# Kernel tuning notes

Measured on AMD Instinct MI355X. Metric: run time of the kernel, lower is better.

The kernel has to match this reference:

```python
import jax, jax.numpy as jnp
import numpy as np

B = 16384
D_VIS, D_LANG, D_STATE = 768, 768, 64
D = 256          # d_model
E = 4            # n_experts
K = 2            # top_k
D_IN = D_VIS + D_LANG + D_STATE
EPS = 1e-5


def layernorm(x, g, b):
    mu = x.mean(-1, keepdims=True)
    var = ((x - mu) ** 2).mean(-1, keepdims=True)
    return g * (x - mu) / jnp.sqrt(var + EPS) + b


def setup_inputs() -> dict:
    key = jax.random.key(0)
    ks = jax.random.split(key, 16)
    s = 0.02
    return {
        "vis": jax.random.normal(ks[0], (B, D_VIS), jnp.float32),
        "lang": jax.random.normal(ks[1], (B, D_LANG), jnp.float32),
        "state": jax.random.normal(ks[2], (B, D_STATE), jnp.float32),
        # fusion: Linear(d_in, d_model) + LayerNorm
        "Wf": jax.random.normal(ks[3], (D_IN, D), jnp.float32) * s,
        "bf": jnp.zeros((D,), jnp.float32),
        "gf": jnp.ones((D,), jnp.float32),
        "bfln": jnp.zeros((D,), jnp.float32),
        # gate (bias=False); random instead of zeros so routing is nontrivial
        "Wg": jax.random.normal(ks[4], (D, E), jnp.float32) * s,
        # stacked experts: Linear(d,2d) -> GELU -> Linear(2d,d) -> GELU -> Linear(d,d), then LN(x + net(x))
        "W1": jax.random.normal(ks[5], (E, D, 2 * D), jnp.float32) * s,
        "b1": jnp.zeros((E, 2 * D), jnp.float32),
        "W2": jax.random.normal(ks[6], (E, 2 * D, D), jnp.float32) * s,
        "b2": jnp.zeros((E, D), jnp.float32),
        "W3": jax.random.normal(ks[7], (E, D, D), jnp.float32) * s,
        "b3": jnp.zeros((E, D), jnp.float32),
        "eg": jnp.ones((E, D), jnp.float32),
        "eb": jnp.zeros((E, D), jnp.float32),
    }


def reference(vis, lang, state, Wf, bf, gf, bfln, Wg, W1, b1, W2, b2, W3, b3, eg, eb):
    gelu = lambda t: jax.nn.gelu(t, approximate=False)
    # fusion: Linear -> LayerNorm -> GELU  (dropout is eval-mode identity)
    x = jnp.concatenate([vis, lang, state], axis=-1) @ Wf + bf   # [B, D]
    x = gelu(layernorm(x, gf, bfln))

    logits = x @ Wg                                              # [B, E]
    all_probs = jax.nn.softmax(logits, axis=-1)
    top_vals, top_idx = jax.lax.top_k(logits, K)                 # [B, K]
    top_w = jax.nn.softmax(top_vals, axis=-1)                    # [B, K]

    # all experts densely (E small); original computes same math per masked subset
    h = gelu(jnp.einsum('bd,edh->beh', x, W1) + b1)              # [B, E, 2D]
    h = gelu(jnp.einsum('beh,ehd->bed', h, W2) + b2)             # [B, E, D]
    h = jnp.einsum('bed,edf->bef', h, W3) + b3                   # [B, E, D]
    y = layernorm(x[:, None, :] + h, eg, eb)                     # [B, E, D]

    # gather selected experts and combine with top-k weights
    y_sel = jnp.take_along_axis(y, top_idx[:, :, None], axis=1)  # [B, K, D]
    out = jnp.einsum('bk,bkd->bd', top_w, y_sel)                 # [B, D]

    # load-balance loss: importance x load
    counts = jnp.zeros((E,), x.dtype).at[top_idx.reshape(-1)].add(1.0)
    f_i = counts / (B * K)
    lb_loss = E * jnp.sum(f_i * all_probs.mean(0))
    return out, lb_loss
```

## Files before the change

### kernel.cpp

```cpp
#include <hip/hip_runtime.h>
#include <math.h>


typedef unsigned short u16;
typedef unsigned int u32;
typedef __attribute__((ext_vector_type(8))) short bf16x8;
typedef __attribute__((ext_vector_type(4))) float f32x4;

__device__ __forceinline__ float bf2f(u16 u) {
    union { u32 i; float f; } v; v.i = ((u32)u) << 16; return v.f;
}
__device__ __forceinline__ u16 f2bf(float f) {
    union { float f; u32 i; } v; v.f = f;
    u32 x = v.i;
    return (u16)((x + 0x7fffu + ((x >> 16) & 1u)) >> 16);
}
__device__ __forceinline__ float gelu_fast(float x) {
    float t = x * (1.59576912f + 0.07135481f * x * x);
    return x / (1.f + __expf(-t));
}
__device__ __forceinline__ u32 pk2(u32 f0, u32 f1) {
    return __builtin_amdgcn_perm(f1, f0, 0x07060302);
}

typedef __attribute__((address_space(1))) void GV;
typedef __attribute__((address_space(3))) void SV;
__device__ __forceinline__ void gldlds(const void* g, void* l) {
    __builtin_amdgcn_global_load_lds((GV*)g, (SV*)l, 16, 0, 0);
}

#define SEG_WF  409600
#define SEG_W1  524288
#define SEG_W2  524288
#define SEG_W3  262144
#define PREP_ITEMS (SEG_WF + SEG_W1 + SEG_W2 + SEG_W3 + 8)

__global__ __launch_bounds__(256) void prep_kernel(
    const float* __restrict__ Wf, const float* __restrict__ W1, const float* __restrict__ W2,
    const float* __restrict__ W3,
    u16* __restrict__ wft, u16* __restrict__ w1t, u16* __restrict__ w2t, u16* __restrict__ w3t,
    float* __restrict__ lbacc) {
    int idx = blockIdx.x * 256 + threadIdx.x;
    if (idx < SEG_WF) {
        int n = idx / 1600, k = idx % 1600;
        wft[idx] = f2bf(Wf[(size_t)k * 256 + n]);
        return;
    }
    idx -= SEG_WF;
    if (idx < SEG_W1) {
        int e = idx >> 17, r = idx & 131071;
        int n = r >> 8, k = r & 255;
        w1t[idx] = f2bf(W1[(size_t)e * 131072 + (size_t)k * 512 + n]);
        return;
    }
    idx -= SEG_W1;
    if (idx < SEG_W2) {
        int e = idx >> 17, r = idx & 131071;
        int n = r >> 9, k = r & 511;
        w2t[idx] = f2bf(W2[(size_t)e * 131072 + (size_t)k * 256 + n]);
        return;
    }
    idx -= SEG_W2;
    if (idx < SEG_W3) {
        int e = idx >> 16, r = idx & 65535;
        int n = r >> 8, k = r & 255;
        w3t[idx] = f2bf(W3[(size_t)e * 65536 + (size_t)k * 256 + n]);
        return;
    }
    idx -= SEG_W3;
    if (idx < 8) lbacc[idx] = 0.0f;
}

__global__ __launch_bounds__(256) void fusion_kernel(
    const float* __restrict__ vis, const float* __restrict__ lang, const float* __restrict__ state,
    const u16* __restrict__ BT, const float* __restrict__ bfv_, const float* __restrict__ gf,
    const float* __restrict__ bfln, const float* __restrict__ Wg,
    u16* __restrict__ xbf, float* __restrict__ wr, float* __restrict__ lbacc) {
    __shared__ __align__(16) u32 Af[2][2048];
    __shared__ __align__(16) u16 Bs[2][16384];
    int tid = threadIdx.x, w = tid >> 6, lane = tid & 63, quad = lane >> 4, l16 = lane & 15;
    int m0 = blockIdx.x * 32;
    f32x4 acc[2][4] = {};

    auto stageAB = [&](int kit, int buf) {
        const float* base; int ld;
        if (kit < 12)      { base = vis + kit * 64;          ld = 768; }
        else if (kit < 24) { base = lang + (kit - 12) * 64;  ld = 768; }
        else               { base = state;                   ld = 64; }
        base += (size_t)m0 * ld;
#pragma unroll
        for (int i = 0; i < 2; ++i) {
            int s = i * 256 + tid, m = s >> 4, c = s & 15;
            gldlds(base + (size_t)m * ld + ((c ^ (m & 15)) << 2), &Af[buf][s * 4]);
        }
#pragma unroll
        for (int i = 0; i < 8; ++i) {
            int s = i * 256 + tid, n = s >> 3, c = s & 7;
            gldlds(BT + (size_t)n * 1600 + kit * 64 + ((c ^ (n & 7)) << 3), &Bs[buf][s * 8]);
        }
    };
    auto comp = [&](int buf) {
#pragma unroll
        for (int ks = 0; ks < 2; ++ks) {
            bf16x8 av[2];
#pragma unroll
            for (int mt = 0; mt < 2; ++mt) {
                int m = mt * 16 + l16;
                int c0 = ks * 8 + quad * 2;
                const u32* rowp = &Af[buf][m * 64];
                uint4 f0 = *(const uint4*)(rowp + ((c0 ^ (m & 15)) << 2));
                uint4 f1 = *(const uint4*)(rowp + (((c0 + 1) ^ (m & 15)) << 2));
                union { u32 u[4]; bf16x8 v; } pk;
                pk.u[0] = pk2(f0.x, f0.y); pk.u[1] = pk2(f0.z, f0.w);
                pk.u[2] = pk2(f1.x, f1.y); pk.u[3] = pk2(f1.z, f1.w);
                av[mt] = pk.v;
            }
#pragma unroll
            for (int nt = 0; nt < 4; ++nt) {
                int n = w * 64 + nt * 16 + l16;
                bf16x8 b = *(const bf16x8*)(&Bs[buf][n * 64 + (((ks * 4 + quad) ^ (n & 7)) << 3)]);
#pragma unroll
                for (int mt = 0; mt < 2; ++mt)
                    acc[mt][nt] = __builtin_amdgcn_mfma_f32_16x16x32_bf16(av[mt], b, acc[mt][nt], 0, 0, 0);
            }
        }
    };

    stageAB(0, 0);
    for (int k = 0; k < 25; ++k) {
        __syncthreads();
        if (k < 24) stageAB(k + 1, (k + 1) & 1);
        comp(k & 1);
    }
    u32* SC = (u32*)(&Bs[1][0]);
    float2* red  = (float2*)SC;
    float*  muv  = (float*)(SC + 256);
    float*  rsv  = (float*)(SC + 288);
    float*  gred = (float*)(SC + 512);
    float*  sacc = (float*)(SC + 1024);

    float bv[4], gvv[4], blv[4]; float4 wgv[4];
#pragma unroll
    for (int nt = 0; nt < 4; ++nt) {
        int col = w * 64 + nt * 16 + l16;
        bv[nt] = bfv_[col]; gvv[nt] = gf[col]; blv[nt] = bfln[col];
        wgv[nt] = *(const float4*)(Wg + col * 4);
    }
    if (tid < 8) sacc[tid] = 0.f;
#pragma unroll
    for (int mt = 0; mt < 2; ++mt)
#pragma unroll
        for (int r = 0; r < 4; ++r) {
            float ss = 0.f, qq = 0.f;
#pragma unroll
            for (int nt = 0; nt < 4; ++nt) {
                float v = acc[mt][nt][r] + bv[nt];
                acc[mt][nt][r] = v;
                ss += v; qq += v * v;
            }
#pragma unroll
            for (int d = 1; d < 16; d <<= 1) { ss += __shfl_xor(ss, d); qq += __shfl_xor(qq, d); }
            if (l16 == 0) red[w * 32 + mt * 16 + quad * 4 + r] = make_float2(ss, qq);
        }
    __syncthreads();
    if (tid < 32) {
        float ss = 0.f, qq = 0.f;
#pragma unroll
        for (int ww = 0; ww < 4; ++ww) { float2 t = red[ww * 32 + tid]; ss += t.x; qq += t.y; }
        float mu = ss * (1.f / 256.f);
        float var = qq * (1.f / 256.f) - mu * mu;
        muv[tid] = mu;
        rsv[tid] = 1.f / sqrtf(var + 1e-5f);
    }
    __syncthreads();
#pragma unroll
    for (int mt = 0; mt < 2; ++mt)
#pragma unroll
        for (int r = 0; r < 4; ++r) {
            int rl = mt * 16 + quad * 4 + r;
            float mu = muv[rl], rs = rsv[rl];
#pragma unroll
            for (int nt = 0; nt < 4; ++nt) {
                int col = w * 64 + nt * 16 + l16;
                float t = (acc[mt][nt][r] - mu) * rs * gvv[nt] + blv[nt];
                float g = gelu_fast(t);
                acc[mt][nt][r] = g;
                xbf[(size_t)(m0 + rl) * 256 + col] = f2bf(g);
            }
        }
#pragma unroll
    for (int mt = 0; mt < 2; ++mt)
#pragma unroll
        for (int r = 0; r < 4; ++r) {
            int rl = mt * 16 + quad * 4 + r;
            float p0 = 0.f, p1 = 0.f, p2 = 0.f, p3 = 0.f;
#pragma unroll
            for (int nt = 0; nt < 4; ++nt) {
                float g = acc[mt][nt][r];
                p0 += g * wgv[nt].x; p1 += g * wgv[nt].y;
                p2 += g * wgv[nt].z; p3 += g * wgv[nt].w;
            }
#pragma unroll
            for (int d = 1; d < 16; d <<= 1) {
                p0 += __shfl_xor(p0, d); p1 += __shfl_xor(p1, d);
                p2 += __shfl_xor(p2, d); p3 += __shfl_xor(p3, d);
            }
            if (l16 == 0) {
                float* gp = gred + w * 128 + rl * 4;
                gp[0] = p0; gp[1] = p1; gp[2] = p2; gp[3] = p3;
            }
        }
    __syncthreads();
    if (tid < 32) {
        int row = tid;
        float lg[4];
#pragma unroll
        for (int e = 0; e < 4; ++e)
            lg[e] = gred[row * 4 + e] + gred[128 + row * 4 + e] +
                    gred[256 + row * 4 + e] + gred[384 + row * 4 + e];
        float mx = fmaxf(fmaxf(lg[0], lg[1]), fmaxf(lg[2], lg[3]));
        float ex[4]; float Z = 0.f;
#pragma unroll
        for (int e = 0; e < 4; ++e) { ex[e] = expf(lg[e] - mx); Z += ex[e]; }
        int i0 = 0; float v0 = lg[0];
#pragma unroll
        for (int e = 1; e < 4; ++e) if (lg[e] > v0) { v0 = lg[e]; i0 = e; }
        int i1 = -1; float v1 = -1e30f;
#pragma unroll
        for (int e = 0; e < 4; ++e) if (e != i0 && lg[e] > v1) { v1 = lg[e]; i1 = e; }
        float t = expf(v1 - v0);
        float wA = 1.f / (1.f + t), wB = t / (1.f + t);
        float w4[4] = {0.f, 0.f, 0.f, 0.f};
        w4[i0] = wA; w4[i1] = wB;
#pragma unroll
        for (int e = 0; e < 4; ++e) wr[(size_t)(m0 + row) * 4 + e] = w4[e];
#pragma unroll
        for (int e = 0; e < 4; ++e) atomicAdd(&sacc[e], ex[e] / Z);
        atomicAdd(&sacc[4 + i0], 1.f);
        atomicAdd(&sacc[4 + i1], 1.f);
    }
    __syncthreads();
    if (tid < 8) atomicAdd(lbacc + tid, sacc[tid]);
}

template<int KITS>
__global__ __launch_bounds__(256) void expert_kernel(
    const u16* __restrict__ A, int lda, long aE,
    const u16* __restrict__ BT, long bE,
    const float* __restrict__ bias, int biasE,
    u16* __restrict__ outp, int ldo, long oE) {
    __shared__ __align__(16) u16 As[2][4096];
    __shared__ __align__(16) u16 Bs[2][8192];
    int tid = threadIdx.x, w = tid >> 6, lane = tid & 63, quad = lane >> 4, l16 = lane & 15;
    int m0 = blockIdx.x * 64;
    int n0 = blockIdx.y * 128;
    int e = blockIdx.z;
    const u16* Ag = A + (size_t)e * aE + (size_t)m0 * lda;
    const u16* Bg = BT + (size_t)e * bE + (size_t)n0 * lda;
    f32x4 acc[4][2] = {};

    auto stage = [&](int kit, int buf) {
#pragma unroll
        for (int i = 0; i < 2; ++i) {
            int s = i * 256 + tid, m = s >> 3, c = s & 7;
            gldlds(Ag + (size_t)m * lda + kit * 64 + ((c ^ (m & 7)) << 3), &As[buf][s * 8]);
        }
#pragma unroll
        for (int i = 0; i < 4; ++i) {
            int s = i * 256 + tid, n = s >> 3, c = s & 7;
            gldlds(Bg + (size_t)n * lda + kit * 64 + ((c ^ (n & 7)) << 3), &Bs[buf][s * 8]);
        }
    };
    auto comp = [&](int buf) {
#pragma unroll
        for (int ks = 0; ks < 2; ++ks) {
            bf16x8 av[4];
#pragma unroll
            for (int mt = 0; mt < 4; ++mt) {
                int m = mt * 16 + l16;
                av[mt] = *(const bf16x8*)(&As[buf][m * 64 + (((ks * 4 + quad) ^ (m & 7)) << 3)]);
            }
#pragma unroll
            for (int nt = 0; nt < 2; ++nt) {
                int n = w * 32 + nt * 16 + l16;
                bf16x8 b = *(const bf16x8*)(&Bs[buf][n * 64 + (((ks * 4 + quad) ^ (n & 7)) << 3)]);
#pragma unroll
                for (int mt = 0; mt < 4; ++mt)
                    acc[mt][nt] = __builtin_amdgcn_mfma_f32_16x16x32_bf16(av[mt], b, acc[mt][nt], 0, 0, 0);
            }
        }
    };

    stage(0, 0);
    for (int k = 0; k < KITS; ++k) {
        __syncthreads();
        if (k + 1 < KITS) stage(k + 1, (k + 1) & 1);
        comp(k & 1);
    }

#pragma unroll
    for (int nt = 0; nt < 2; ++nt) {
        int col = n0 + w * 32 + nt * 16 + l16;
        float bvv = bias[e * biasE + col];
#pragma unroll
        for (int mt = 0; mt < 4; ++mt)
#pragma unroll
            for (int r = 0; r < 4; ++r) {
                int row = m0 + mt * 16 + quad * 4 + r;
                outp[(size_t)e * oE + (size_t)row * ldo + col] = f2bf(gelu_fast(acc[mt][nt][r] + bvv));
            }
    }
}

__global__ __launch_bounds__(256) void combine_kernel(
    const u16* __restrict__ h2, const u16* __restrict__ W3T,
    const float* __restrict__ b3, const float* __restrict__ eg, const float* __restrict__ eb,
    const u16* __restrict__ xbf, const float* __restrict__ wr,
    const float* __restrict__ lbacc, float* __restrict__ outp) {
    __shared__ __align__(16) u16 Bs[2][16384];
    __shared__ float wl[128];
    __shared__ float2 red[128];
    __shared__ float muv[32], rsv[32];
    int tid = threadIdx.x, w = tid >> 6, lane = tid & 63, quad = lane >> 4, l16 = lane & 15;
    int m0 = blockIdx.x * 32;
    if (blockIdx.x == 0 && tid == 0) {
        float lb = 0.f;
#pragma unroll
        for (int e = 0; e < 4; ++e)
            lb += (lbacc[4 + e] / 32768.f) * (lbacc[e] / 16384.f);
        outp[4194304] = 4.f * lb;
    }
    u16 xr[2][2][4];
    u16 xrr[2][4][4];
#pragma unroll
    for (int mt = 0; mt < 2; ++mt)
#pragma unroll
        for (int r = 0; r < 4; ++r) {
            int row = m0 + mt * 16 + quad * 4 + r;
#pragma unroll
            for (int nt = 0; nt < 4; ++nt)
                xrr[mt][nt][r] = xbf[(size_t)row * 256 + w * 64 + nt * 16 + l16];
        }
    (void)xr;
    if (tid < 128) wl[tid] = wr[(size_t)m0 * 4 + tid];

    auto stageB = [&](int u, int buf) {
        int e = u >> 2, kit = u & 3;
        const u16* Bg = W3T + (size_t)e * 65536;
#pragma unroll
        for (int i = 0; i < 8; ++i) {
            int s = i * 256 + tid, n = s >> 3, c = s & 7;
            gldlds(Bg + (size_t)n * 256 + kit * 64 + ((c ^ (n & 7)) << 3), &Bs[buf][s * 8]);
        }
    };
    uint4 aR[2][2][2];
    auto loadA = [&](int u, int ring) {
        int e = u >> 2, kit = u & 3;
#pragma unroll
        for (int mt = 0; mt < 2; ++mt) {
            const u16* p = h2 + ((size_t)e * 16384 + m0 + mt * 16 + l16) * 256 + kit * 64 + quad * 8;
            aR[ring][mt][0] = *(const uint4*)p;
            aR[ring][mt][1] = *(const uint4*)(p + 16);
        }
    };

    f32x4 oacc[2][4] = {};
    f32x4 acc[2][4] = {};
    stageB(0, 0); loadA(0, 0);
#pragma unroll 4
    for (int u = 0; u < 16; ++u) {
        __syncthreads();
        if (u < 15) { stageB(u + 1, (u + 1) & 1); loadA(u + 1, (u + 1) & 1); }
#pragma unroll
        for (int ks = 0; ks < 2; ++ks) {
#pragma unroll
            for (int nt = 0; nt < 4; ++nt) {
                int n = w * 64 + nt * 16 + l16;
                bf16x8 b = *(const bf16x8*)(&Bs[u & 1][n * 64 + (((ks * 4 + quad) ^ (n & 7)) << 3)]);
#pragma unroll
                for (int mt = 0; mt < 2; ++mt) {
                    union { uint4 u4; bf16x8 v; } av; av.u4 = aR[u & 1][mt][ks];
                    acc[mt][nt] = __builtin_amdgcn_mfma_f32_16x16x32_bf16(av.v, b, acc[mt][nt], 0, 0, 0);
                }
            }
        }
        if ((u & 3) == 3) {
            int e = u >> 2;
            float b3v[4], egv[4], ebv[4];
#pragma unroll
            for (int nt = 0; nt < 4; ++nt) {
                int col = w * 64 + nt * 16 + l16;
                b3v[nt] = b3[e * 256 + col]; egv[nt] = eg[e * 256 + col]; ebv[nt] = eb[e * 256 + col];
            }
#pragma unroll
            for (int mt = 0; mt < 2; ++mt)
#pragma unroll
                for (int r = 0; r < 4; ++r) {
                    int rl = mt * 16 + quad * 4 + r;
                    float ss = 0.f, qq = 0.f;
#pragma unroll
                    for (int nt = 0; nt < 4; ++nt) {
                        float v = acc[mt][nt][r] + b3v[nt] + bf2f(xrr[mt][nt][r]);
                        acc[mt][nt][r] = v;
                        ss += v; qq += v * v;
                    }
#pragma unroll
                    for (int d = 1; d < 16; d <<= 1) { ss += __shfl_xor(ss, d); qq += __shfl_xor(qq, d); }
                    if (l16 == 0) red[w * 32 + rl] = make_float2(ss, qq);
                }
            __syncthreads();
            if (tid < 32) {
                float ss = 0.f, qq = 0.f;
#pragma unroll
                for (int ww = 0; ww < 4; ++ww) { float2 t = red[ww * 32 + tid]; ss += t.x; qq += t.y; }
                float mu = ss * (1.f / 256.f);
                float var = qq * (1.f / 256.f) - mu * mu;
                muv[tid] = mu;
                rsv[tid] = 1.f / sqrtf(var + 1e-5f);
            }
            __syncthreads();
#pragma unroll
            for (int mt = 0; mt < 2; ++mt)
#pragma unroll
                for (int r = 0; r < 4; ++r) {
                    int rl = mt * 16 + quad * 4 + r;
                    float mu = muv[rl], rs = rsv[rl], we = wl[rl * 4 + e];
#pragma unroll
                    for (int nt = 0; nt < 4; ++nt) {
                        float y = (acc[mt][nt][r] - mu) * rs * egv[nt] + ebv[nt];
                        oacc[mt][nt][r] += we * y;
                        acc[mt][nt][r] = 0.f;
                    }
                }
        }
    }
#pragma unroll
    for (int mt = 0; mt < 2; ++mt)
#pragma unroll
        for (int r = 0; r < 4; ++r) {
            int rl = mt * 16 + quad * 4 + r;
#pragma unroll
            for (int nt = 0; nt < 4; ++nt) {
                int col = w * 64 + nt * 16 + l16;
                outp[(size_t)(m0 + rl) * 256 + col] = oacc[mt][nt][r];
            }
        }
}

extern "C" void kernel_launch(void* const* d_in, const int* in_sizes, int n_in,
                              void* d_out, int out_size, void* d_ws, size_t ws_size,
                              hipStream_t stream) {
    const float* vis   = (const float*)d_in[0];
    const float* lang  = (const float*)d_in[1];
    const float* state = (const float*)d_in[2];
    const float* Wf    = (const float*)d_in[3];
    const float* bf_   = (const float*)d_in[4];
    const float* gf    = (const float*)d_in[5];
    const float* bfln  = (const float*)d_in[6];
    const float* Wg    = (const float*)d_in[7];
    const float* W1    = (const float*)d_in[8];
    const float* b1    = (const float*)d_in[9];
    const float* W2    = (const float*)d_in[10];
    const float* b2    = (const float*)d_in[11];
    const float* W3    = (const float*)d_in[12];
    const float* b3    = (const float*)d_in[13];
    const float* eg    = (const float*)d_in[14];
    const float* eb    = (const float*)d_in[15];
    float* outp = (float*)d_out;

    char* ws = (char*)d_ws;
    size_t off = 0;
    float* lbacc = (float*)(ws + off); off += 256;
    u16* WFT  = (u16*)(ws + off); off += 819200UL;
    u16* W1T  = (u16*)(ws + off); off += 1048576UL;
    u16* W2T  = (u16*)(ws + off); off += 1048576UL;
    u16* W3T  = (u16*)(ws + off); off += 524288UL;
    u16* XBF  = (u16*)(ws + off); off += 8388608UL;
    float* WR = (float*)(ws + off); off += 262144UL;
    u16* H1   = (u16*)(ws + off); off += 67108864UL;
    u16* H2   = (u16*)(ws + off); off += 33554432UL;
    if (ws_size < off) return;

    int prep_blocks = (PREP_ITEMS + 255) / 256;
    prep_kernel<<<prep_blocks, 256, 0, stream>>>(Wf, W1, W2, W3, WFT, W1T, W2T, W3T, lbacc);
    fusion_kernel<<<512, 256, 0, stream>>>(vis, lang, state, WFT, bf_, gf, bfln, Wg,
                                           XBF, WR, lbacc);
    expert_kernel<4><<<dim3(256, 4, 4), 256, 0, stream>>>(
        XBF, 256, 0L, W1T, 131072L, b1, 512, H1, 512, 8388608L);
    expert_kernel<8><<<dim3(256, 2, 4), 256, 0, stream>>>(
        H1, 512, 8388608L, W2T, 131072L, b2, 256, H2, 256, 4194304L);
    combine_kernel<<<512, 256, 0, stream>>>(H2, W3T, b3, eg, eb, XBF, WR, lbacc, outp);
}
```

Before: 342.6 us.

## Split-K fusion GEMM with separate reduce, larger tiles, drop double buffering

Splits the fusion GEMM into a 128x128-tiled split-K kernel that writes bf16 partials, plus a separate reduce kernel that sums the partials and applies bias, LayerNorm, GELU and the gate softmax. The expert GEMMs move to 128x128 tiles with a 2x2 warp layout, and the combine kernel to 64-row tiles with A staged through LDS. All kernels drop the double-buffered prefetch in favour of single-buffered load-then-compute. The aim is more reuse per block and more parallelism in the fusion step. The cost is about 40 MB of extra partial-sum traffic, loss of load/compute overlap, and bf16 rounding of the partials before they are summed.

Result: no change. 336.8 us (-1.7%).

```diff
diff --git a/kernel.cpp b/kernel.cpp
--- a/kernel.cpp
+++ b/kernel.cpp
@@ -22,7 +22,6 @@
 __device__ __forceinline__ u32 pk2(u32 f0, u32 f1) {
     return __builtin_amdgcn_perm(f1, f0, 0x07060302);
 }
-
 typedef __attribute__((address_space(1))) void GV;
 typedef __attribute__((address_space(3))) void SV;
 __device__ __forceinline__ void gldlds(const void* g, void* l) {
@@ -71,43 +70,42 @@
     if (idx < 8) lbacc[idx] = 0.0f;
 }
 
-__global__ __launch_bounds__(256) void fusion_kernel(
+__global__ __launch_bounds__(256) void fusion_gemm(
     const float* __restrict__ vis, const float* __restrict__ lang, const float* __restrict__ state,
-    const u16* __restrict__ BT, const float* __restrict__ bfv_, const float* __restrict__ gf,
-    const float* __restrict__ bfln, const float* __restrict__ Wg,
-    u16* __restrict__ xbf, float* __restrict__ wr, float* __restrict__ lbacc) {
-    __shared__ __align__(16) u32 Af[2][2048];
-    __shared__ __align__(16) u16 Bs[2][16384];
+    const u16* __restrict__ BT, u16* __restrict__ part) {
+    __shared__ __align__(16) u32 Af[8192];
+    __shared__ __align__(16) u16 Bs[8192];
     int tid = threadIdx.x, w = tid >> 6, lane = tid & 63, quad = lane >> 4, l16 = lane & 15;
-    int m0 = blockIdx.x * 32;
-    f32x4 acc[2][4] = {};
-
-    auto stageAB = [&](int kit, int buf) {
-        const float* base; int ld;
-        if (kit < 12)      { base = vis + kit * 64;          ld = 768; }
-        else if (kit < 24) { base = lang + (kit - 12) * 64;  ld = 768; }
-        else               { base = state;                   ld = 64; }
-        base += (size_t)m0 * ld;
-#pragma unroll
-        for (int i = 0; i < 2; ++i) {
+    int wm = w >> 1, wn = w & 1;
+    int m0 = blockIdx.x * 128, n0 = blockIdx.y * 128, ks0 = blockIdx.z * 5;
+    f32x4 acc[4][4] = {};
+
+    for (int kit = 0; kit < 5; ++kit) {
+        int kg = ks0 + kit;
+        const float* base; int ld, koff;
+        if (kg < 12)      { base = vis;   ld = 768; koff = kg * 64; }
+        else if (kg < 24) { base = lang;  ld = 768; koff = (kg - 12) * 64; }
+        else              { base = state; ld = 64;  koff = 0; }
+        __syncthreads();
+#pragma unroll
+        for (int i = 0; i < 8; ++i) {
             int s = i * 256 + tid, m = s >> 4, c = s & 15;
-            gldlds(base + (size_t)m * ld + ((c ^ (m & 15)) << 2), &Af[buf][s * 4]);
-        }
-#pragma unroll
-        for (int i = 0; i < 8; ++i) {
+            gldlds(base + (size_t)(m0 + m) * ld + koff + ((c ^ (m & 15)) << 2), &Af[s * 4]);
+        }
+#pragma unroll
+        for (int i = 0; i < 4; ++i) {
             int s = i * 256 + tid, n = s >> 3, c = s & 7;
-            gldlds(BT + (size_t)n * 1600 + kit * 64 + ((c ^ (n & 7)) << 3), &Bs[buf][s * 8]);
-        }
-    };
-    auto comp = [&](int buf) {
+            gldlds(BT + (size_t)(n0 + n) * 1600 + kg * 64 + ((c ^ (n & 7)) << 3), &Bs[s * 8]);
+        }
+        __syncthreads();
 #pragma unroll
         for (int ks = 0; ks < 2; ++ks) {
-            bf16x8 av[2];
-#pragma unroll
-            for (int mt = 0; mt < 2; ++mt) {
-                int m = mt * 16 + l16;
+            bf16x8 av[4];
+#pragma unroll
+            for (int mt = 0; mt < 4; ++mt) {
+                int m = wm * 64 + mt * 16 + l16;
                 int c0 = ks * 8 + quad * 2;
-                const u32* rowp = &Af[buf][m * 64];
+                const u32* rowp = &Af[m * 64];
                 uint4 f0 = *(const uint4*)(rowp + ((c0 ^ (m & 15)) << 2));
                 uint4 f1 = *(const uint4*)(rowp + (((c0 + 1) ^ (m & 15)) << 2));
                 union { u32 u[4]; bf16x8 v; } pk;
@@ -117,107 +115,91 @@
             }
 #pragma unroll
             for (int nt = 0; nt < 4; ++nt) {
-                int n = w * 64 + nt * 16 + l16;
-                bf16x8 b = *(const bf16x8*)(&Bs[buf][n * 64 + (((ks * 4 + quad) ^ (n & 7)) << 3)]);
-#pragma unroll
-                for (int mt = 0; mt < 2; ++mt)
+                int n = wn * 64 + nt * 16 + l16;
+                bf16x8 b = *(const bf16x8*)(&Bs[n * 64 + (((ks * 4 + quad) ^ (n & 7)) << 3)]);
+#pragma unroll
+                for (int mt = 0; mt < 4; ++mt)
                     acc[mt][nt] = __builtin_amdgcn_mfma_f32_16x16x32_bf16(av[mt], b, acc[mt][nt], 0, 0, 0);
             }
         }
-    };
-
-    stageAB(0, 0);
-    for (int k = 0; k < 25; ++k) {
-        __syncthreads();
-        if (k < 24) stageAB(k + 1, (k + 1) & 1);
-        comp(k & 1);
-    }
-    u32* SC = (u32*)(&Bs[1][0]);
-    float2* red  = (float2*)SC;
-    float*  muv  = (float*)(SC + 256);
-    float*  rsv  = (float*)(SC + 288);
-    float*  gred = (float*)(SC + 512);
-    float*  sacc = (float*)(SC + 1024);
-
-    float bv[4], gvv[4], blv[4]; float4 wgv[4];
-#pragma unroll
-    for (int nt = 0; nt < 4; ++nt) {
-        int col = w * 64 + nt * 16 + l16;
-        bv[nt] = bfv_[col]; gvv[nt] = gf[col]; blv[nt] = bfln[col];
-        wgv[nt] = *(const float4*)(Wg + col * 4);
-    }
+    }
+    u16* pp = part + (size_t)blockIdx.z * 4194304;
+#pragma unroll
+    for (int mt = 0; mt < 4; ++mt)
+#pragma unroll
+        for (int r = 0; r < 4; ++r) {
+            int row = m0 + wm * 64 + mt * 16 + quad * 4 + r;
+#pragma unroll
+            for (int nt = 0; nt < 4; ++nt) {
+                int col = n0 + wn * 64 + nt * 16 + l16;
+                pp[(size_t)row * 256 + col] = f2bf(acc[mt][nt][r]);
+            }
+        }
+}
+
+__global__ __launch_bounds__(256) void freduce_kernel(
+    const u16* __restrict__ part, const float* __restrict__ bfv, const float* __restrict__ gf,
+    const float* __restrict__ bfln, const float* __restrict__ Wg,
+    u16* __restrict__ xbf, float* __restrict__ wr, float* __restrict__ lbacc) {
+    __shared__ float sacc[8];
+    int tid = threadIdx.x;
     if (tid < 8) sacc[tid] = 0.f;
-#pragma unroll
-    for (int mt = 0; mt < 2; ++mt)
-#pragma unroll
-        for (int r = 0; r < 4; ++r) {
-            float ss = 0.f, qq = 0.f;
-#pragma unroll
-            for (int nt = 0; nt < 4; ++nt) {
-                float v = acc[mt][nt][r] + bv[nt];
-                acc[mt][nt][r] = v;
-                ss += v; qq += v * v;
-            }
-#pragma unroll
-            for (int d = 1; d < 16; d <<= 1) { ss += __shfl_xor(ss, d); qq += __shfl_xor(qq, d); }
-            if (l16 == 0) red[w * 32 + mt * 16 + quad * 4 + r] = make_float2(ss, qq);
-        }
     __syncthreads();
-    if (tid < 32) {
-        float ss = 0.f, qq = 0.f;
-#pragma unroll
-        for (int ww = 0; ww < 4; ++ww) { float2 t = red[ww * 32 + tid]; ss += t.x; qq += t.y; }
-        float mu = ss * (1.f / 256.f);
-        float var = qq * (1.f / 256.f) - mu * mu;
-        muv[tid] = mu;
-        rsv[tid] = 1.f / sqrtf(var + 1e-5f);
-    }
-    __syncthreads();
-#pragma unroll
-    for (int mt = 0; mt < 2; ++mt)
-#pragma unroll
-        for (int r = 0; r < 4; ++r) {
-            int rl = mt * 16 + quad * 4 + r;
-            float mu = muv[rl], rs = rsv[rl];
-#pragma unroll
-            for (int nt = 0; nt < 4; ++nt) {
-                int col = w * 64 + nt * 16 + l16;
-                float t = (acc[mt][nt][r] - mu) * rs * gvv[nt] + blv[nt];
-                float g = gelu_fast(t);
-                acc[mt][nt][r] = g;
-                xbf[(size_t)(m0 + rl) * 256 + col] = f2bf(g);
-            }
-        }
-#pragma unroll
-    for (int mt = 0; mt < 2; ++mt)
-#pragma unroll
-        for (int r = 0; r < 4; ++r) {
-            int rl = mt * 16 + quad * 4 + r;
-            float p0 = 0.f, p1 = 0.f, p2 = 0.f, p3 = 0.f;
-#pragma unroll
-            for (int nt = 0; nt < 4; ++nt) {
-                float g = acc[mt][nt][r];
-                p0 += g * wgv[nt].x; p1 += g * wgv[nt].y;
-                p2 += g * wgv[nt].z; p3 += g * wgv[nt].w;
-            }
-#pragma unroll
-            for (int d = 1; d < 16; d <<= 1) {
-                p0 += __shfl_xor(p0, d); p1 += __shfl_xor(p1, d);
-                p2 += __shfl_xor(p2, d); p3 += __shfl_xor(p3, d);
-            }
-            if (l16 == 0) {
-                float* gp = gred + w * 128 + rl * 4;
-                gp[0] = p0; gp[1] = p1; gp[2] = p2; gp[3] = p3;
-            }
-        }
-    __syncthreads();
-    if (tid < 32) {
-        int row = tid;
-        float lg[4];
-#pragma unroll
-        for (int e = 0; e < 4; ++e)
-            lg[e] = gred[row * 4 + e] + gred[128 + row * 4 + e] +
-                    gred[256 + row * 4 + e] + gred[384 + row * 4 + e];
+    int r = tid >> 3, cg = tid & 7;
+    int row = blockIdx.x * 32 + r;
+    int c0 = cg * 32;
+    float x[32] = {};
+#pragma unroll
+    for (int s = 0; s < 5; ++s) {
+        const u16* p = part + (size_t)s * 4194304 + (size_t)row * 256 + c0;
+#pragma unroll
+        for (int v = 0; v < 4; ++v) {
+            uint4 q = *(const uint4*)(p + v * 8);
+            u32 wsv[4] = {q.x, q.y, q.z, q.w};
+#pragma unroll
+            for (int h = 0; h < 4; ++h) {
+                x[v * 8 + h * 2]     += bf2f((u16)(wsv[h] & 0xffff));
+                x[v * 8 + h * 2 + 1] += bf2f((u16)(wsv[h] >> 16));
+            }
+        }
+    }
+    float ss = 0.f, qq = 0.f;
+#pragma unroll
+    for (int j = 0; j < 32; ++j) {
+        x[j] += bfv[c0 + j];
+        ss += x[j]; qq += x[j] * x[j];
+    }
+#pragma unroll
+    for (int d = 1; d < 8; d <<= 1) { ss += __shfl_xor(ss, d); qq += __shfl_xor(qq, d); }
+    float mu = ss * (1.f / 256.f);
+    float var = qq * (1.f / 256.f) - mu * mu;
+    float rs = 1.f / sqrtf(var + 1e-5f);
+    float p0 = 0.f, p1 = 0.f, p2 = 0.f, p3 = 0.f;
+    float g[32];
+#pragma unroll
+    for (int j = 0; j < 32; ++j) {
+        float t = (x[j] - mu) * rs * gf[c0 + j] + bfln[c0 + j];
+        float gg = gelu_fast(t);
+        g[j] = gg;
+        float4 wg = *(const float4*)(Wg + (size_t)(c0 + j) * 4);
+        p0 += gg * wg.x; p1 += gg * wg.y; p2 += gg * wg.z; p3 += gg * wg.w;
+    }
+#pragma unroll
+    for (int v = 0; v < 4; ++v) {
+        uint4 o;
+        o.x = (u32)f2bf(g[v*8+0]) | ((u32)f2bf(g[v*8+1]) << 16);
+        o.y = (u32)f2bf(g[v*8+2]) | ((u32)f2bf(g[v*8+3]) << 16);
+        o.z = (u32)f2bf(g[v*8+4]) | ((u32)f2bf(g[v*8+5]) << 16);
+        o.w = (u32)f2bf(g[v*8+6]) | ((u32)f2bf(g[v*8+7]) << 16);
+        *(uint4*)(xbf + (size_t)row * 256 + c0 + v * 8) = o;
+    }
+#pragma unroll
+    for (int d = 1; d < 8; d <<= 1) {
+        p0 += __shfl_xor(p0, d); p1 += __shfl_xor(p1, d);
+        p2 += __shfl_xor(p2, d); p3 += __shfl_xor(p3, d);
+    }
+    if (cg == 0) {
+        float lg[4] = {p0, p1, p2, p3};
         float mx = fmaxf(fmaxf(lg[0], lg[1]), fmaxf(lg[2], lg[3]));
         float ex[4]; float Z = 0.f;
 #pragma unroll
@@ -233,7 +215,7 @@
         float w4[4] = {0.f, 0.f, 0.f, 0.f};
         w4[i0] = wA; w4[i1] = wB;
 #pragma unroll
-        for (int e = 0; e < 4; ++e) wr[(size_t)(m0 + row) * 4 + e] = w4[e];
+        for (int e = 0; e < 4; ++e) wr[(size_t)row * 4 + e] = w4[e];
 #pragma unroll
         for (int e = 0; e < 4; ++e) atomicAdd(&sacc[e], ex[e] / Z);
         atomicAdd(&sacc[4 + i0], 1.f);
@@ -249,64 +231,56 @@
     const u16* __restrict__ BT, long bE,
     const float* __restrict__ bias, int biasE,
     u16* __restrict__ outp, int ldo, long oE) {
-    __shared__ __align__(16) u16 As[2][4096];
-    __shared__ __align__(16) u16 Bs[2][8192];
+    __shared__ __align__(16) u16 As[8192];
+    __shared__ __align__(16) u16 Bs[8192];
     int tid = threadIdx.x, w = tid >> 6, lane = tid & 63, quad = lane >> 4, l16 = lane & 15;
-    int m0 = blockIdx.x * 64;
-    int n0 = blockIdx.y * 128;
+    int wm = w >> 1, wn = w & 1;
+    int m0 = blockIdx.x * 128, n0 = blockIdx.y * 128;
     int e = blockIdx.z;
     const u16* Ag = A + (size_t)e * aE + (size_t)m0 * lda;
     const u16* Bg = BT + (size_t)e * bE + (size_t)n0 * lda;
-    f32x4 acc[4][2] = {};
-
-    auto stage = [&](int kit, int buf) {
-#pragma unroll
-        for (int i = 0; i < 2; ++i) {
+    f32x4 acc[4][4] = {};
+
+    for (int kit = 0; kit < KITS; ++kit) {
+        __syncthreads();
+#pragma unroll
+        for (int i = 0; i < 4; ++i) {
             int s = i * 256 + tid, m = s >> 3, c = s & 7;
-            gldlds(Ag + (size_t)m * lda + kit * 64 + ((c ^ (m & 7)) << 3), &As[buf][s * 8]);
+            gldlds(Ag + (size_t)m * lda + kit * 64 + ((c ^ (m & 7)) << 3), &As[s * 8]);
         }
 #pragma unroll
         for (int i = 0; i < 4; ++i) {
             int s = i * 256 + tid, n = s >> 3, c = s & 7;
-            gldlds(Bg + (size_t)n * lda + kit * 64 + ((c ^ (n & 7)) << 3), &Bs[buf][s * 8]);
-        }
-    };
-    auto comp = [&](int buf) {
+            gldlds(Bg + (size_t)n * lda + kit * 64 + ((c ^ (n & 7)) << 3), &Bs[s * 8]);
+        }
+        __syncthreads();
 #pragma unroll
         for (int ks = 0; ks < 2; ++ks) {
             bf16x8 av[4];
 #pragma unroll
             for (int mt = 0; mt < 4; ++mt) {
-                int m = mt * 16 + l16;
-                av[mt] = *(const bf16x8*)(&As[buf][m * 64 + (((ks * 4 + quad) ^ (m & 7)) << 3)]);
-            }
-#pragma unroll
-            for (int nt = 0; nt < 2; ++nt) {
-                int n = w * 32 + nt * 16 + l16;
-                bf16x8 b = *(const bf16x8*)(&Bs[buf][n * 64 + (((ks * 4 + quad) ^ (n & 7)) << 3)]);
+                int m = wm * 64 + mt * 16 + l16;
+                av[mt] = *(const bf16x8*)(&As[m * 64 + (((ks * 4 + quad) ^ (m & 7)) << 3)]);
+            }
+#pragma unroll
+            for (int nt = 0; nt < 4; ++nt) {
+                int n = wn * 64 + nt * 16 + l16;
+                bf16x8 b = *(const bf16x8*)(&Bs[n * 64 + (((ks * 4 + quad) ^ (n & 7)) << 3)]);
 #pragma unroll
                 for (int mt = 0; mt < 4; ++mt)
                     acc[mt][nt] = __builtin_amdgcn_mfma_f32_16x16x32_bf16(av[mt], b, acc[mt][nt], 0, 0, 0);
             }
         }
-    };
-
-    stage(0, 0);
-    for (int k = 0; k < KITS; ++k) {
-        __syncthreads();
-        if (k + 1 < KITS) stage(k + 1, (k + 1) & 1);
-        comp(k & 1);
-    }
-
-#pragma unroll
-    for (int nt = 0; nt < 2; ++nt) {
-        int col = n0 + w * 32 + nt * 16 + l16;
+    }
+#pragma unroll
+    for (int nt = 0; nt < 4; ++nt) {
+        int col = n0 + wn * 64 + nt * 16 + l16;
         float bvv = bias[e * biasE + col];
 #pragma unroll
         for (int mt = 0; mt < 4; ++mt)
 #pragma unroll
             for (int r = 0; r < 4; ++r) {
-                int row = m0 + mt * 16 + quad * 4 + r;
+                int row = m0 + wm * 64 + mt * 16 + quad * 4 + r;
                 outp[(size_t)e * oE + (size_t)row * ldo + col] = f2bf(gelu_fast(acc[mt][nt][r] + bvv));
             }
     }
@@ -317,12 +291,13 @@
     const float* __restrict__ b3, const float* __restrict__ eg, const float* __restrict__ eb,
     const u16* __restrict__ xbf, const float* __restrict__ wr,
     const float* __restrict__ lbacc, float* __restrict__ outp) {
-    __shared__ __align__(16) u16 Bs[2][16384];
-    __shared__ float wl[128];
-    __shared__ float2 red[128];
-    __shared__ float muv[32], rsv[32];
+    __shared__ __align__(16) u16 As[4096];
+    __shared__ __align__(16) u16 Bs[16384];
+    __shared__ float wl[256];
+    __shared__ float2 red[256];
+    __shared__ float muv[64], rsv[64];
     int tid = threadIdx.x, w = tid >> 6, lane = tid & 63, quad = lane >> 4, l16 = lane & 15;
-    int m0 = blockIdx.x * 32;
+    int m0 = blockIdx.x * 64;
     if (blockIdx.x == 0 && tid == 0) {
         float lb = 0.f;
 #pragma unroll
@@ -330,10 +305,9 @@
             lb += (lbacc[4 + e] / 32768.f) * (lbacc[e] / 16384.f);
         outp[4194304] = 4.f * lb;
     }
-    u16 xr[2][2][4];
-    u16 xrr[2][4][4];
-#pragma unroll
-    for (int mt = 0; mt < 2; ++mt)
+    u16 xrr[4][4][4];
+#pragma unroll
+    for (int mt = 0; mt < 4; ++mt)
 #pragma unroll
         for (int r = 0; r < 4; ++r) {
             int row = m0 + mt * 16 + quad * 4 + r;
@@ -341,101 +315,93 @@
             for (int nt = 0; nt < 4; ++nt)
                 xrr[mt][nt][r] = xbf[(size_t)row * 256 + w * 64 + nt * 16 + l16];
         }
-    (void)xr;
-    if (tid < 128) wl[tid] = wr[(size_t)m0 * 4 + tid];
-
-    auto stageB = [&](int u, int buf) {
-        int e = u >> 2, kit = u & 3;
+    wl[tid] = wr[(size_t)m0 * 4 + tid];
+
+    f32x4 oacc[4][4] = {};
+#pragma unroll 1
+    for (int e = 0; e < 4; ++e) {
+        const u16* Ag = h2 + ((size_t)e * 16384 + m0) * 256;
         const u16* Bg = W3T + (size_t)e * 65536;
-#pragma unroll
-        for (int i = 0; i < 8; ++i) {
-            int s = i * 256 + tid, n = s >> 3, c = s & 7;
-            gldlds(Bg + (size_t)n * 256 + kit * 64 + ((c ^ (n & 7)) << 3), &Bs[buf][s * 8]);
-        }
-    };
-    uint4 aR[2][2][2];
-    auto loadA = [&](int u, int ring) {
-        int e = u >> 2, kit = u & 3;
-#pragma unroll
-        for (int mt = 0; mt < 2; ++mt) {
-            const u16* p = h2 + ((size_t)e * 16384 + m0 + mt * 16 + l16) * 256 + kit * 64 + quad * 8;
-            aR[ring][mt][0] = *(const uint4*)p;
-            aR[ring][mt][1] = *(const uint4*)(p + 16);
-        }
-    };
-
-    f32x4 oacc[2][4] = {};
-    f32x4 acc[2][4] = {};
-    stageB(0, 0); loadA(0, 0);
-#pragma unroll 4
-    for (int u = 0; u < 16; ++u) {
-        __syncthreads();
-        if (u < 15) { stageB(u + 1, (u + 1) & 1); loadA(u + 1, (u + 1) & 1); }
-#pragma unroll
-        for (int ks = 0; ks < 2; ++ks) {
-#pragma unroll
-            for (int nt = 0; nt < 4; ++nt) {
-                int n = w * 64 + nt * 16 + l16;
-                bf16x8 b = *(const bf16x8*)(&Bs[u & 1][n * 64 + (((ks * 4 + quad) ^ (n & 7)) << 3)]);
-#pragma unroll
-                for (int mt = 0; mt < 2; ++mt) {
-                    union { uint4 u4; bf16x8 v; } av; av.u4 = aR[u & 1][mt][ks];
-                    acc[mt][nt] = __builtin_amdgcn_mfma_f32_16x16x32_bf16(av.v, b, acc[mt][nt], 0, 0, 0);
+        f32x4 acc[4][4] = {};
+        for (int kit = 0; kit < 4; ++kit) {
+            __syncthreads();
+#pragma unroll
+            for (int i = 0; i < 2; ++i) {
+                int s = i * 256 + tid, m = s >> 3, c = s & 7;
+                gldlds(Ag + (size_t)m * 256 + kit * 64 + ((c ^ (m & 7)) << 3), &As[s * 8]);
+            }
+#pragma unroll
+            for (int i = 0; i < 8; ++i) {
+                int s = i * 256 + tid, n = s >> 3, c = s & 7;
+                gldlds(Bg + (size_t)n * 256 + kit * 64 + ((c ^ (n & 7)) << 3), &Bs[s * 8]);
+            }
+            __syncthreads();
+#pragma unroll
+            for (int ks = 0; ks < 2; ++ks) {
+                bf16x8 av[4];
+#pragma unroll
+                for (int mt = 0; mt < 4; ++mt) {
+                    int m = mt * 16 + l16;
+                    av[mt] = *(const bf16x8*)(&As[m * 64 + (((ks * 4 + quad) ^ (m & 7)) << 3)]);
                 }
-            }
-        }
-        if ((u & 3) == 3) {
-            int e = u >> 2;
-            float b3v[4], egv[4], ebv[4];
-#pragma unroll
-            for (int nt = 0; nt < 4; ++nt) {
-                int col = w * 64 + nt * 16 + l16;
-                b3v[nt] = b3[e * 256 + col]; egv[nt] = eg[e * 256 + col]; ebv[nt] = eb[e * 256 + col];
-            }
-#pragma unroll
-            for (int mt = 0; mt < 2; ++mt)
-#pragma unroll
-                for (int r = 0; r < 4; ++r) {
-                    int rl = mt * 16 + quad * 4 + r;
-                    float ss = 0.f, qq = 0.f;
-#pragma unroll
-                    for (int nt = 0; nt < 4; ++nt) {
-                        float v = acc[mt][nt][r] + b3v[nt] + bf2f(xrr[mt][nt][r]);
-                        acc[mt][nt][r] = v;
-                        ss += v; qq += v * v;
-                    }
-#pragma unroll
-                    for (int d = 1; d < 16; d <<= 1) { ss += __shfl_xor(ss, d); qq += __shfl_xor(qq, d); }
-                    if (l16 == 0) red[w * 32 + rl] = make_float2(ss, qq);
+#pragma unroll
+                for (int nt = 0; nt < 4; ++nt) {
+                    int n = w * 64 + nt * 16 + l16;
+                    bf16x8 b = *(const bf16x8*)(&Bs[n * 64 + (((ks * 4 + quad) ^ (n & 7)) << 3)]);
+#pragma unroll
+                    for (int mt = 0; mt < 4; ++mt)
+                        acc[mt][nt] = __builtin_amdgcn_mfma_f32_16x16x32_bf16(av[mt], b, acc[mt][nt], 0, 0, 0);
                 }
-            __syncthreads();
-            if (tid < 32) {
+            }
+        }
+        float b3v[4], egv[4], ebv[4];
+#pragma unroll
+        for (int nt = 0; nt < 4; ++nt) {
+            int col = w * 64 + nt * 16 + l16;
+            b3v[nt] = b3[e * 256 + col]; egv[nt] = eg[e * 256 + col]; ebv[nt] = eb[e * 256 + col];
+        }
+#pragma unroll
+        for (int mt = 0; mt < 4; ++mt)
+#pragma unroll
+            for (int r = 0; r < 4; ++r) {
+                int rl = mt * 16 + quad * 4 + r;
                 float ss = 0.f, qq = 0.f;
 #pragma unroll
-                for (int ww = 0; ww < 4; ++ww) { float2 t = red[ww * 32 + tid]; ss += t.x; qq += t.y; }
-                float mu = ss * (1.f / 256.f);
-                float var = qq * (1.f / 256.f) - mu * mu;
-                muv[tid] = mu;
-                rsv[tid] = 1.f / sqrtf(var + 1e-5f);
-            }
-            __syncthreads();
-#pragma unroll
-            for (int mt = 0; mt < 2; ++mt)
-#pragma unroll
-                for (int r = 0; r < 4; ++r) {
-                    int rl = mt * 16 + quad * 4 + r;
-                    float mu = muv[rl], rs = rsv[rl], we = wl[rl * 4 + e];
-#pragma unroll
-                    for (int nt = 0; nt < 4; ++nt) {
-                        float y = (acc[mt][nt][r] - mu) * rs * egv[nt] + ebv[nt];
-                        oacc[mt][nt][r] += we * y;
-                        acc[mt][nt][r] = 0.f;
-                    }
+                for (int nt = 0; nt < 4; ++nt) {
+                    float v = acc[mt][nt][r] + b3v[nt] + bf2f(xrr[mt][nt][r]);
+                    acc[mt][nt][r] = v;
+                    ss += v; qq += v * v;
                 }
-        }
-    }
-#pragma unroll
-    for (int mt = 0; mt < 2; ++mt)
+#pragma unroll
+                for (int d = 1; d < 16; d <<= 1) { ss += __shfl_xor(ss, d); qq += __shfl_xor(qq, d); }
+                if (l16 == 0) red[w * 64 + rl] = make_float2(ss, qq);
+            }
+        __syncthreads();
+        if (tid < 64) {
+            float ss = 0.f, qq = 0.f;
+#pragma unroll
+            for (int ww = 0; ww < 4; ++ww) { float2 t = red[ww * 64 + tid]; ss += t.x; qq += t.y; }
+            float mu = ss * (1.f / 256.f);
+            float var = qq * (1.f / 256.f) - mu * mu;
+            muv[tid] = mu;
+            rsv[tid] = 1.f / sqrtf(var + 1e-5f);
+        }
+        __syncthreads();
+#pragma unroll
+        for (int mt = 0; mt < 4; ++mt)
+#pragma unroll
+            for (int r = 0; r < 4; ++r) {
+                int rl = mt * 16 + quad * 4 + r;
+                float mu = muv[rl], rs = rsv[rl], we = wl[rl * 4 + e];
+#pragma unroll
+                for (int nt = 0; nt < 4; ++nt) {
+                    float y = (acc[mt][nt][r] - mu) * rs * egv[nt] + ebv[nt];
+                    oacc[mt][nt][r] += we * y;
+                }
+            }
+    }
+#pragma unroll
+    for (int mt = 0; mt < 4; ++mt)
 #pragma unroll
         for (int r = 0; r < 4; ++r) {
             int rl = mt * 16 + quad * 4 + r;
@@ -479,15 +445,16 @@
     float* WR = (float*)(ws + off); off += 262144UL;
     u16* H1   = (u16*)(ws + off); off += 67108864UL;
     u16* H2   = (u16*)(ws + off); off += 33554432UL;
+    u16* PART = (u16*)(ws + off); off += 41943040UL;
     if (ws_size < off) return;
 
     int prep_blocks = (PREP_ITEMS + 255) / 256;
     prep_kernel<<<prep_blocks, 256, 0, stream>>>(Wf, W1, W2, W3, WFT, W1T, W2T, W3T, lbacc);
-    fusion_kernel<<<512, 256, 0, stream>>>(vis, lang, state, WFT, bf_, gf, bfln, Wg,
-                                           XBF, WR, lbacc);
-    expert_kernel<4><<<dim3(256, 4, 4), 256, 0, stream>>>(
+    fusion_gemm<<<dim3(128, 2, 5), 256, 0, stream>>>(vis, lang, state, WFT, PART);
+    freduce_kernel<<<512, 256, 0, stream>>>(PART, bf_, gf, bfln, Wg, XBF, WR, lbacc);
+    expert_kernel<4><<<dim3(128, 4, 4), 256, 0, stream>>>(
         XBF, 256, 0L, W1T, 131072L, b1, 512, H1, 512, 8388608L);
-    expert_kernel<8><<<dim3(256, 2, 4), 256, 0, stream>>>(
+    expert_kernel<8><<<dim3(128, 2, 4), 256, 0, stream>>>(
         H1, 512, 8388608L, W2T, 131072L, b2, 256, H2, 256, 4194304L);
-    combine_kernel<<<512, 256, 0, stream>>>(H2, W3T, b3, eg, eb, XBF, WR, lbacc, outp);
-}
+    combine_kernel<<<256, 256, 0, stream>>>(H2, W3T, b3, eg, eb, XBF, WR, lbacc, outp);
+}
```
